# Kernel optimization log

Measured on AMD Instinct MI355X. Metric: run time of the kernel, lower is better.

The kernel has to match this reference:

```python
import jax, jax.numpy as jnp
import numpy as np


def setup_inputs() -> dict:
    key = jax.random.key(0)
    k0, k1, k2, k3 = jax.random.split(key, 4)
    B, S, D, F, E = 2, 2048, 1024, 4096, 8
    hidden_states = jax.random.normal(k0, (B, S, D), dtype=jnp.float32)
    Wr = jax.random.normal(k1, (E, D), dtype=jnp.float32) * 0.02   # router Linear weight [E, D]
    W1 = jax.random.normal(k2, (E, D, F), dtype=jnp.float32) * 0.02  # expert w1 (transposed torch layout)
    W2 = jax.random.normal(k3, (E, F, D), dtype=jnp.float32) * 0.02  # expert w2
    return {"hidden_states": hidden_states, "Wr": Wr, "W1": W1, "W2": W2, "top_k": 2}


def reference(hidden_states, Wr, W1, W2, top_k):
    # hidden_states: [B, S, D]; Wr: [E, D]; W1: [E, D, F]; W2: [E, F, D]
    E = Wr.shape[0]
    dt = hidden_states.dtype

    # Router: logits -> top-k expert indices. NOTE: the original module computes
    # softmax routing weights over the top-k logits but never applies them in the
    # combine step, so the output is an UNWEIGHTED sum over selected experts.
    router_logits = jnp.einsum('bsd,ed->bse', hidden_states, Wr)
    _, topk_idx = jax.lax.top_k(router_logits, top_k)            # [B, S, K]

    # mask[b,s,e] = 1 if expert e is in token (b,s)'s top-k (indices are distinct)
    mask = (jax.nn.one_hot(topk_idx, E, dtype=dt).sum(axis=-2) > 0).astype(dt)  # [B, S, E]

    # Dense per-expert FFN (SiLU MLP, no bias, dropout=identity in eval):
    h = jax.nn.silu(jnp.einsum('bsd,edf->bsef', hidden_states, W1))  # [B, S, E, F]
    y = jnp.einsum('bsef,efd->bsed', h, W2)                          # [B, S, E, D]

    # Combine: unweighted sum over selected experts (faithful to source)
    return jnp.einsum('bsed,bse->bsd', y, mask)
```

## Files before the change

### kernel.cpp

```cpp
#include <hip/hip_runtime.h>
#include <hip/hip_bf16.h>
#include <stdint.h>

#define TOKENS 4096
#define DDIM 1024
#define FDIM 4096
#define NEXP 8
#define BM 128
#define BN 256
#define BK 64
#define MT (TOKENS / BM)

typedef __attribute__((ext_vector_type(4))) float f32x4;
typedef __attribute__((ext_vector_type(8))) short short8;

__device__ __forceinline__ unsigned short f2bf(float f) {
    union { float f; uint32_t u; } v; v.f = f;
    uint32_t u = v.u;
    return (unsigned short)((u + 0x7fff + ((u >> 16) & 1)) >> 16);
}

#define BARRIER() asm volatile("s_barrier" ::: "memory")
#define WAIT_VM0() asm volatile("s_waitcnt vmcnt(0)" ::: "memory")
#define GLDS(SRC, DST) __builtin_amdgcn_global_load_lds( \
    (const __attribute__((address_space(1))) void*)(SRC), \
    (__attribute__((address_space(3))) void*)(DST), 16, 0, 0)

__global__ __launch_bounds__(256) void cvt_x(const float* __restrict__ x,
                                             unsigned short* __restrict__ xb, int n) {
    int i = (blockIdx.x * 256 + threadIdx.x) * 8;
    if (i >= n) return;
    float4 a = *(const float4*)(x + i);
    float4 b = *(const float4*)(x + i + 4);
    short8 o;
    o[0] = f2bf(a.x); o[1] = f2bf(a.y); o[2] = f2bf(a.z); o[3] = f2bf(a.w);
    o[4] = f2bf(b.x); o[5] = f2bf(b.y); o[6] = f2bf(b.z); o[7] = f2bf(b.w);
    *(short8*)(xb + i) = o;
}

__global__ __launch_bounds__(256) void transpose_cvt(const float* __restrict__ in,
                                                     unsigned short* __restrict__ out,
                                                     int R, int C) {
    __shared__ float tile[32][33];
    int e = blockIdx.z;
    int r0 = blockIdx.y * 32, c0 = blockIdx.x * 32;
    const float* src = in + (size_t)e * R * C;
    unsigned short* dst = out + (size_t)e * R * C;
    int t = threadIdx.x;
    int rr = t >> 3;
    int cc = (t & 7) * 4;
    float4 v = *(const float4*)(src + (size_t)(r0 + rr) * C + c0 + cc);
    tile[rr][cc + 0] = v.x; tile[rr][cc + 1] = v.y;
    tile[rr][cc + 2] = v.z; tile[rr][cc + 3] = v.w;
    __syncthreads();
    int oc = rr;
    int orr = cc;
    ushort4 o;
    o.x = f2bf(tile[orr + 0][oc]);
    o.y = f2bf(tile[orr + 1][oc]);
    o.z = f2bf(tile[orr + 2][oc]);
    o.w = f2bf(tile[orr + 3][oc]);
    *(ushort4*)(dst + (size_t)(c0 + oc) * R + r0 + orr) = o;
}

__global__ __launch_bounds__(256) void router(const float* __restrict__ x,
                                              const float* __restrict__ wr,
                                              int* __restrict__ cnt,
                                              int* __restrict__ list) {
    __shared__ float wl[NEXP * DDIM];
    int t = threadIdx.x;
    for (int i = t; i < NEXP * DDIM; i += 256) wl[i] = wr[i];
    __syncthreads();
    int tok = blockIdx.x * 4 + (t >> 6);
    int lane = t & 63;
    float acc[NEXP];
#pragma unroll
    for (int e = 0; e < NEXP; e++) acc[e] = 0.f;
    const float* xr = x + (size_t)tok * DDIM;
    for (int d = lane; d < DDIM; d += 64) {
        float xv = xr[d];
#pragma unroll
        for (int e = 0; e < NEXP; e++) acc[e] += xv * wl[e * DDIM + d];
    }
#pragma unroll
    for (int e = 0; e < NEXP; e++) {
#pragma unroll
        for (int off = 32; off; off >>= 1) acc[e] += __shfl_xor(acc[e], off);
    }
    if (lane == 0) {
        int e1 = 0; float v1 = acc[0];
        for (int e = 1; e < NEXP; e++) if (acc[e] > v1) { v1 = acc[e]; e1 = e; }
        int e2 = -1; float v2 = -1e30f;
        for (int e = 0; e < NEXP; e++) if (e != e1 && acc[e] > v2) { v2 = acc[e]; e2 = e; }
        int p1 = atomicAdd(&cnt[e1], 1);
        list[e1 * TOKENS + p1] = tok;
        int p2 = atomicAdd(&cnt[e2], 1);
        list[e2 * TOKENS + p2] = tok;
    }
}

__global__ void prefix(const int* __restrict__ cnt, int* __restrict__ off) {
    if (threadIdx.x == 0) {
        int s = 0;
        for (int e = 0; e < NEXP; e++) { off[e] = s; s += cnt[e]; }
    }
}

template <bool GATHER_A, bool SILU>
__global__ __launch_bounds__(512, 2) void gemm_moe2(
    const unsigned short* __restrict__ Abase,
    const unsigned short* __restrict__ Wt,
    const int* __restrict__ cnt, const int* __restrict__ off,
    const int* __restrict__ list,
    unsigned short* __restrict__ Hout,
    float* __restrict__ Yout,
    int KD, int NDIM) {
    __shared__ alignas(16) unsigned short As[2][BM * BK];
    __shared__ alignas(16) unsigned short Bs[2][BN * BK];

    int gx = gridDim.x;
    int flat = blockIdx.y * gx + blockIdx.x;
    int nwg = gx * (int)gridDim.y;
    int q = nwg >> 3, r = nwg & 7;
    int xcd = flat & 7, idx = flat >> 3;
    int swz = (xcd < r) ? (xcd * (q + 1) + idx) : (r * (q + 1) + (xcd - r) * q + idx);
    int bx = swz % gx, by = swz / gx;

    int e = bx / MT, mtile = bx % MT;
    int n_e = cnt[e];
    int m0 = mtile * BM;
    if (m0 >= n_e) return;
    int base = off[e];
    int n0 = by * BN;

    int t = threadIdx.x;
    int lane = t & 63;
    int wid = t >> 6;
    int wm = wid >> 2, wn = wid & 3;
    int r16 = lane & 15, g = lane >> 4;

    const unsigned short* pA[2];
    const unsigned short* pB[4];
    int ldsA[2], ldsB[4];
#pragma unroll
    for (int i = 0; i < 2; i++) {
        int c = i * 512 + t;
        int row = c >> 3, cc = c & 7;
        int arow = m0 + row; if (arow >= n_e) arow = n_e - 1;
        size_t grow = GATHER_A ? (size_t)list[e * TOKENS + arow] : (size_t)(base + arow);
        pA[i] = Abase + grow * (size_t)KD + ((cc ^ (row & 7)) << 3);
        ldsA[i] = c * 16;
    }
#pragma unroll
    for (int i = 0; i < 4; i++) {
        int c = i * 512 + t;
        int row = c >> 3, cc = c & 7;
        pB[i] = Wt + ((size_t)e * NDIM + n0 + row) * (size_t)KD + ((cc ^ (row & 7)) << 3);
        ldsB[i] = c * 16;
    }

    f32x4 acc[4][4];
#pragma unroll
    for (int i = 0; i < 4; i++)
#pragma unroll
        for (int j = 0; j < 4; j++) acc[i][j] = f32x4{0.f, 0.f, 0.f, 0.f};

#define FRAG(TILE, ROW, KC) (*(const short8*)&(TILE)[(ROW) * BK + ((((KC)) ^ ((ROW) & 7)) << 3)])

#pragma unroll
    for (int i = 0; i < 4; i++) { GLDS(pB[i], (char*)Bs[0] + ldsB[i]); pB[i] += BK; }
#pragma unroll
    for (int i = 0; i < 2; i++) { GLDS(pA[i], (char*)As[0] + ldsA[i]); pA[i] += BK; }
    WAIT_VM0();
    BARRIER();

    const int NT = KD / BK;
    for (int tk = 0; tk < NT; ++tk) {
        const unsigned short* Ac = As[tk & 1];
        const unsigned short* Bc = Bs[tk & 1];
        char* Ad = (char*)As[(tk & 1) ^ 1];
        char* Bd = (char*)Bs[(tk & 1) ^ 1];
        const bool pf = (tk + 1 < NT);

        short8 b0, b1, b2, b3, a0, a1;
        b0 = FRAG(Bc, wn * 64 + 0 * 16 + r16, g);
        b1 = FRAG(Bc, wn * 64 + 1 * 16 + r16, g);
        b2 = FRAG(Bc, wn * 64 + 2 * 16 + r16, g);
        b3 = FRAG(Bc, wn * 64 + 3 * 16 + r16, g);
        a0 = FRAG(Ac, wm * 64 + 0 * 16 + r16, g);
        a1 = FRAG(Ac, wm * 64 + 1 * 16 + r16, g);
        if (pf) { GLDS(pB[0], Bd + ldsB[0]); pB[0] += BK; GLDS(pB[1], Bd + ldsB[1]); pB[1] += BK; }
        BARRIER();
        __builtin_amdgcn_s_setprio(1);
        acc[0][0] = __builtin_amdgcn_mfma_f32_16x16x32_bf16(a0, b0, acc[0][0], 0, 0, 0);
        acc[0][1] = __builtin_amdgcn_mfma_f32_16x16x32_bf16(a0, b1, acc[0][1], 0, 0, 0);
        acc[0][2] = __builtin_amdgcn_mfma_f32_16x16x32_bf16(a0, b2, acc[0][2], 0, 0, 0);
        acc[0][3] = __builtin_amdgcn_mfma_f32_16x16x32_bf16(a0, b3, acc[0][3], 0, 0, 0);
        acc[1][0] = __builtin_amdgcn_mfma_f32_16x16x32_bf16(a1, b0, acc[1][0], 0, 0, 0);
        acc[1][1] = __builtin_amdgcn_mfma_f32_16x16x32_bf16(a1, b1, acc[1][1], 0, 0, 0);
        acc[1][2] = __builtin_amdgcn_mfma_f32_16x16x32_bf16(a1, b2, acc[1][2], 0, 0, 0);
        acc[1][3] = __builtin_amdgcn_mfma_f32_16x16x32_bf16(a1, b3, acc[1][3], 0, 0, 0);
        __builtin_amdgcn_s_setprio(0);
        BARRIER();
        a0 = FRAG(Ac, wm * 64 + 2 * 16 + r16, g);
        a1 = FRAG(Ac, wm * 64 + 3 * 16 + r16, g);
        if (pf) { GLDS(pB[2], Bd + ldsB[2]); pB[2] += BK; GLDS(pB[3], Bd + ldsB[3]); pB[3] += BK; }
        BARRIER();
        __builtin_amdgcn_s_setprio(1);
        acc[2][0] = __builtin_amdgcn_mfma_f32_16x16x32_bf16(a0, b0, acc[2][0], 0, 0, 0);
        acc[2][1] = __builtin_amdgcn_mfma_f32_16x16x32_bf16(a0, b1, acc[2][1], 0, 0, 0);
        acc[2][2] = __builtin_amdgcn_mfma_f32_16x16x32_bf16(a0, b2, acc[2][2], 0, 0, 0);
        acc[2][3] = __builtin_amdgcn_mfma_f32_16x16x32_bf16(a0, b3, acc[2][3], 0, 0, 0);
        acc[3][0] = __builtin_amdgcn_mfma_f32_16x16x32_bf16(a1, b0, acc[3][0], 0, 0, 0);
        acc[3][1] = __builtin_amdgcn_mfma_f32_16x16x32_bf16(a1, b1, acc[3][1], 0, 0, 0);
        acc[3][2] = __builtin_amdgcn_mfma_f32_16x16x32_bf16(a1, b2, acc[3][2], 0, 0, 0);
        acc[3][3] = __builtin_amdgcn_mfma_f32_16x16x32_bf16(a1, b3, acc[3][3], 0, 0, 0);
        __builtin_amdgcn_s_setprio(0);
        BARRIER();
        b0 = FRAG(Bc, wn * 64 + 0 * 16 + r16, 4 + g);
        b1 = FRAG(Bc, wn * 64 + 1 * 16 + r16, 4 + g);
        b2 = FRAG(Bc, wn * 64 + 2 * 16 + r16, 4 + g);
        b3 = FRAG(Bc, wn * 64 + 3 * 16 + r16, 4 + g);
        a0 = FRAG(Ac, wm * 64 + 0 * 16 + r16, 4 + g);
        a1 = FRAG(Ac, wm * 64 + 1 * 16 + r16, 4 + g);
        if (pf) { GLDS(pA[0], Ad + ldsA[0]); pA[0] += BK; GLDS(pA[1], Ad + ldsA[1]); pA[1] += BK; }
        BARRIER();
        __builtin_amdgcn_s_setprio(1);
        acc[0][0] = __builtin_amdgcn_mfma_f32_16x16x32_bf16(a0, b0, acc[0][0], 0, 0, 0);
        acc[0][1] = __builtin_amdgcn_mfma_f32_16x16x32_bf16(a0, b1, acc[0][1], 0, 0, 0);
        acc[0][2] = __builtin_amdgcn_mfma_f32_16x16x32_bf16(a0, b2, acc[0][2], 0, 0, 0);
        acc[0][3] = __builtin_amdgcn_mfma_f32_16x16x32_bf16(a0, b3, acc[0][3], 0, 0, 0);
        acc[1][0] = __builtin_amdgcn_mfma_f32_16x16x32_bf16(a1, b0, acc[1][0], 0, 0, 0);
        acc[1][1] = __builtin_amdgcn_mfma_f32_16x16x32_bf16(a1, b1, acc[1][1], 0, 0, 0);
        acc[1][2] = __builtin_amdgcn_mfma_f32_16x16x32_bf16(a1, b2, acc[1][2], 0, 0, 0);
        acc[1][3] = __builtin_amdgcn_mfma_f32_16x16x32_bf16(a1, b3, acc[1][3], 0, 0, 0);
        __builtin_amdgcn_s_setprio(0);
        BARRIER();
        a0 = FRAG(Ac, wm * 64 + 2 * 16 + r16, 4 + g);
        a1 = FRAG(Ac, wm * 64 + 3 * 16 + r16, 4 + g);
        BARRIER();
        __builtin_amdgcn_s_setprio(1);
        acc[2][0] = __builtin_amdgcn_mfma_f32_16x16x32_bf16(a0, b0, acc[2][0], 0, 0, 0);
        acc[2][1] = __builtin_amdgcn_mfma_f32_16x16x32_bf16(a0, b1, acc[2][1], 0, 0, 0);
        acc[2][2] = __builtin_amdgcn_mfma_f32_16x16x32_bf16(a0, b2, acc[2][2], 0, 0, 0);
        acc[2][3] = __builtin_amdgcn_mfma_f32_16x16x32_bf16(a0, b3, acc[2][3], 0, 0, 0);
        acc[3][0] = __builtin_amdgcn_mfma_f32_16x16x32_bf16(a1, b0, acc[3][0], 0, 0, 0);
        acc[3][1] = __builtin_amdgcn_mfma_f32_16x16x32_bf16(a1, b1, acc[3][1], 0, 0, 0);
        acc[3][2] = __builtin_amdgcn_mfma_f32_16x16x32_bf16(a1, b2, acc[3][2], 0, 0, 0);
        acc[3][3] = __builtin_amdgcn_mfma_f32_16x16x32_bf16(a1, b3, acc[3][3], 0, 0, 0);
        __builtin_amdgcn_s_setprio(0);
        if (pf) WAIT_VM0();
        BARRIER();
    }
#undef FRAG

#pragma unroll
    for (int mi = 0; mi < 4; ++mi) {
#pragma unroll
        for (int nj = 0; nj < 4; ++nj) {
#pragma unroll
            for (int qq = 0; qq < 4; ++qq) {
                int lr = wm * 64 + mi * 16 + g * 4 + qq;
                if (m0 + lr < n_e) {
                    int col = n0 + wn * 64 + nj * 16 + r16;
                    float v = acc[mi][nj][qq];
                    if (SILU) {
                        v = v / (1.f + __expf(-v));
                        Hout[(size_t)(base + m0 + lr) * NDIM + col] = f2bf(v);
                    } else {
                        int tok = list[e * TOKENS + m0 + lr];
                        atomicAdd(&Yout[(size_t)tok * NDIM + col], v);
                    }
                }
            }
        }
    }
}

extern "C" void kernel_launch(void* const* d_in, const int* in_sizes, int n_in,
                              void* d_out, int out_size, void* d_ws, size_t ws_size,
                              hipStream_t stream) {
    const float* X  = (const float*)d_in[0];
    const float* Wr = (const float*)d_in[1];
    const float* W1 = (const float*)d_in[2];
    const float* W2 = (const float*)d_in[3];
    float* Y = (float*)d_out;

    char* ws = (char*)d_ws;
    int* cnt  = (int*)(ws + 0);
    int* off  = (int*)(ws + 128);
    int* list = (int*)(ws + 1024);
    unsigned short* Xb = (unsigned short*)(ws + (1ull << 20));
    unsigned short* WT = (unsigned short*)(ws + (16ull << 20));
    unsigned short* H  = (unsigned short*)(ws + (80ull << 20));

    hipMemsetAsync(d_out, 0, (size_t)out_size * sizeof(float), stream);
    hipMemsetAsync(cnt, 0, 32, stream);

    cvt_x<<<TOKENS * DDIM / (256 * 8), 256, 0, stream>>>(X, Xb, TOKENS * DDIM);
    router<<<TOKENS / 4, 256, 0, stream>>>(X, Wr, cnt, list);
    prefix<<<1, 64, 0, stream>>>(cnt, off);

    transpose_cvt<<<dim3(FDIM / 32, DDIM / 32, NEXP), 256, 0, stream>>>(W1, WT, DDIM, FDIM);
    gemm_moe2<true, true><<<dim3(NEXP * MT, FDIM / BN), 512, 0, stream>>>(
        Xb, WT, cnt, off, list, H, nullptr, DDIM, FDIM);

    transpose_cvt<<<dim3(DDIM / 32, FDIM / 32, NEXP), 256, 0, stream>>>(W2, WT, FDIM, DDIM);
    gemm_moe2<false, false><<<dim3(NEXP * MT, DDIM / BN), 512, 0, stream>>>(
        H, WT, cnt, off, list, nullptr, Y, FDIM, DDIM);
}
```

Measured before the change: 542.7 us.

## Make MoE GEMMs persistent with an atomic work queue over non-empty tiles

Replaces the fixed 2D grid, where most blocks exit early on empty expert tiles, with 512 persistent workgroups. Each one pulls compact tile indices from an atomic counter, and a setup kernel precomputes per-expert tile bases and totals. The tile shrinks from 128x256 to 128x128 with 256 threads. The k-loop becomes simpler: all prefetches are issued at once and there is a single barrier per step. The intent is to remove launch waste and load imbalance. The costs are more weight-tile reloads, since N tiles are smaller, and less overlap between loads and MFMAs.

```diff
diff --git a/kernel.cpp b/kernel.cpp
--- a/kernel.cpp
+++ b/kernel.cpp
@@ -7,9 +7,8 @@
 #define FDIM 4096
 #define NEXP 8
 #define BM 128
-#define BN 256
+#define BN 128
 #define BK 64
-#define MT (TOKENS / BM)
 
 typedef __attribute__((ext_vector_type(4))) float f32x4;
 typedef __attribute__((ext_vector_type(8))) short short8;
@@ -99,182 +98,189 @@
     }
 }
 
-__global__ void prefix(const int* __restrict__ cnt, int* __restrict__ off) {
+__global__ void setup(const int* __restrict__ cnt, int* __restrict__ off,
+                      int* __restrict__ wbA, int* __restrict__ wbB,
+                      int* __restrict__ qctr, int* __restrict__ tot) {
     if (threadIdx.x == 0) {
-        int s = 0;
-        for (int e = 0; e < NEXP; e++) { off[e] = s; s += cnt[e]; }
+        int s = 0, ta = 0, tb = 0;
+        for (int e = 0; e < NEXP; e++) {
+            off[e] = s; s += cnt[e];
+            wbA[e] = ta; wbB[e] = tb;
+            int nt = (cnt[e] + BM - 1) / BM;
+            ta += nt * (FDIM / BN);
+            tb += nt * (DDIM / BN);
+        }
+        wbA[NEXP] = ta; wbB[NEXP] = tb;
+        tot[0] = ta; tot[1] = tb;
+        qctr[0] = 0; qctr[1] = 0;
     }
 }
 
 template <bool GATHER_A, bool SILU>
-__global__ __launch_bounds__(512, 2) void gemm_moe2(
+__global__ __launch_bounds__(256, 2) void gemm_moe3(
     const unsigned short* __restrict__ Abase,
     const unsigned short* __restrict__ Wt,
     const int* __restrict__ cnt, const int* __restrict__ off,
     const int* __restrict__ list,
+    const int* __restrict__ wbase,
+    int* __restrict__ qctr, const int* __restrict__ tot,
     unsigned short* __restrict__ Hout,
     float* __restrict__ Yout,
     int KD, int NDIM) {
     __shared__ alignas(16) unsigned short As[2][BM * BK];
     __shared__ alignas(16) unsigned short Bs[2][BN * BK];
-
-    int gx = gridDim.x;
-    int flat = blockIdx.y * gx + blockIdx.x;
-    int nwg = gx * (int)gridDim.y;
-    int q = nwg >> 3, r = nwg & 7;
-    int xcd = flat & 7, idx = flat >> 3;
-    int swz = (xcd < r) ? (xcd * (q + 1) + idx) : (r * (q + 1) + (xcd - r) * q + idx);
-    int bx = swz % gx, by = swz / gx;
-
-    int e = bx / MT, mtile = bx % MT;
-    int n_e = cnt[e];
-    int m0 = mtile * BM;
-    if (m0 >= n_e) return;
-    int base = off[e];
-    int n0 = by * BN;
+    __shared__ int wsh;
 
     int t = threadIdx.x;
     int lane = t & 63;
     int wid = t >> 6;
-    int wm = wid >> 2, wn = wid & 3;
+    int wm = wid >> 1, wn = wid & 1;
     int r16 = lane & 15, g = lane >> 4;
-
-    const unsigned short* pA[2];
-    const unsigned short* pB[4];
-    int ldsA[2], ldsB[4];
-#pragma unroll
-    for (int i = 0; i < 2; i++) {
-        int c = i * 512 + t;
-        int row = c >> 3, cc = c & 7;
-        int arow = m0 + row; if (arow >= n_e) arow = n_e - 1;
-        size_t grow = GATHER_A ? (size_t)list[e * TOKENS + arow] : (size_t)(base + arow);
-        pA[i] = Abase + grow * (size_t)KD + ((cc ^ (row & 7)) << 3);
-        ldsA[i] = c * 16;
-    }
-#pragma unroll
-    for (int i = 0; i < 4; i++) {
-        int c = i * 512 + t;
-        int row = c >> 3, cc = c & 7;
-        pB[i] = Wt + ((size_t)e * NDIM + n0 + row) * (size_t)KD + ((cc ^ (row & 7)) << 3);
-        ldsB[i] = c * 16;
-    }
-
-    f32x4 acc[4][4];
-#pragma unroll
-    for (int i = 0; i < 4; i++)
-#pragma unroll
-        for (int j = 0; j < 4; j++) acc[i][j] = f32x4{0.f, 0.f, 0.f, 0.f};
+    const int total = *tot;
 
 #define FRAG(TILE, ROW, KC) (*(const short8*)&(TILE)[(ROW) * BK + ((((KC)) ^ ((ROW) & 7)) << 3)])
 
-#pragma unroll
-    for (int i = 0; i < 4; i++) { GLDS(pB[i], (char*)Bs[0] + ldsB[i]); pB[i] += BK; }
-#pragma unroll
-    for (int i = 0; i < 2; i++) { GLDS(pA[i], (char*)As[0] + ldsA[i]); pA[i] += BK; }
-    WAIT_VM0();
-    BARRIER();
-
-    const int NT = KD / BK;
-    for (int tk = 0; tk < NT; ++tk) {
-        const unsigned short* Ac = As[tk & 1];
-        const unsigned short* Bc = Bs[tk & 1];
-        char* Ad = (char*)As[(tk & 1) ^ 1];
-        char* Bd = (char*)Bs[(tk & 1) ^ 1];
-        const bool pf = (tk + 1 < NT);
-
-        short8 b0, b1, b2, b3, a0, a1;
-        b0 = FRAG(Bc, wn * 64 + 0 * 16 + r16, g);
-        b1 = FRAG(Bc, wn * 64 + 1 * 16 + r16, g);
-        b2 = FRAG(Bc, wn * 64 + 2 * 16 + r16, g);
-        b3 = FRAG(Bc, wn * 64 + 3 * 16 + r16, g);
-        a0 = FRAG(Ac, wm * 64 + 0 * 16 + r16, g);
-        a1 = FRAG(Ac, wm * 64 + 1 * 16 + r16, g);
-        if (pf) { GLDS(pB[0], Bd + ldsB[0]); pB[0] += BK; GLDS(pB[1], Bd + ldsB[1]); pB[1] += BK; }
+    for (;;) {
+        if (t == 0) wsh = atomicAdd(qctr, 1);
+        __syncthreads();
+        int w = wsh;
+        if (w >= total) break;
+
+        int e = 0;
+        while (e < NEXP - 1 && w >= wbase[e + 1]) e++;
+        w -= wbase[e];
+        int n_e = cnt[e];
+        int ntm = (n_e + BM - 1) >> 7;
+        int by = w / ntm;
+        int mtile = w - by * ntm;
+        int m0 = mtile * BM;
+        int n0 = by * BN;
+        int base = off[e];
+
+        const unsigned short* pA[4];
+        const unsigned short* pB[4];
+        int ldsA[4], ldsB[4];
+#pragma unroll
+        for (int i = 0; i < 4; i++) {
+            int c = i * 256 + t;
+            int row = c >> 3, cc = c & 7;
+            int arow = m0 + row; if (arow >= n_e) arow = n_e - 1;
+            size_t grow = GATHER_A ? (size_t)list[e * TOKENS + arow] : (size_t)(base + arow);
+            pA[i] = Abase + grow * (size_t)KD + ((cc ^ (row & 7)) << 3);
+            ldsA[i] = c * 16;
+            pB[i] = Wt + ((size_t)e * NDIM + n0 + row) * (size_t)KD + ((cc ^ (row & 7)) << 3);
+            ldsB[i] = c * 16;
+        }
+
+        f32x4 acc[4][4];
+#pragma unroll
+        for (int i = 0; i < 4; i++)
+#pragma unroll
+            for (int j = 0; j < 4; j++) acc[i][j] = f32x4{0.f, 0.f, 0.f, 0.f};
+
+#pragma unroll
+        for (int i = 0; i < 4; i++) { GLDS(pB[i], (char*)Bs[0] + ldsB[i]); pB[i] += BK; }
+#pragma unroll
+        for (int i = 0; i < 4; i++) { GLDS(pA[i], (char*)As[0] + ldsA[i]); pA[i] += BK; }
+        WAIT_VM0();
         BARRIER();
-        __builtin_amdgcn_s_setprio(1);
-        acc[0][0] = __builtin_amdgcn_mfma_f32_16x16x32_bf16(a0, b0, acc[0][0], 0, 0, 0);
-        acc[0][1] = __builtin_amdgcn_mfma_f32_16x16x32_bf16(a0, b1, acc[0][1], 0, 0, 0);
-        acc[0][2] = __builtin_amdgcn_mfma_f32_16x16x32_bf16(a0, b2, acc[0][2], 0, 0, 0);
-        acc[0][3] = __builtin_amdgcn_mfma_f32_16x16x32_bf16(a0, b3, acc[0][3], 0, 0, 0);
-        acc[1][0] = __builtin_amdgcn_mfma_f32_16x16x32_bf16(a1, b0, acc[1][0], 0, 0, 0);
-        acc[1][1] = __builtin_amdgcn_mfma_f32_16x16x32_bf16(a1, b1, acc[1][1], 0, 0, 0);
-        acc[1][2] = __builtin_amdgcn_mfma_f32_16x16x32_bf16(a1, b2, acc[1][2], 0, 0, 0);
-        acc[1][3] = __builtin_amdgcn_mfma_f32_16x16x32_bf16(a1, b3, acc[1][3], 0, 0, 0);
-        __builtin_amdgcn_s_setprio(0);
-        BARRIER();
-        a0 = FRAG(Ac, wm * 64 + 2 * 16 + r16, g);
-        a1 = FRAG(Ac, wm * 64 + 3 * 16 + r16, g);
-        if (pf) { GLDS(pB[2], Bd + ldsB[2]); pB[2] += BK; GLDS(pB[3], Bd + ldsB[3]); pB[3] += BK; }
-        BARRIER();
-        __builtin_amdgcn_s_setprio(1);
-        acc[2][0] = __builtin_amdgcn_mfma_f32_16x16x32_bf16(a0, b0, acc[2][0], 0, 0, 0);
-        acc[2][1] = __builtin_amdgcn_mfma_f32_16x16x32_bf16(a0, b1, acc[2][1], 0, 0, 0);
-        acc[2][2] = __builtin_amdgcn_mfma_f32_16x16x32_bf16(a0, b2, acc[2][2], 0, 0, 0);
-        acc[2][3] = __builtin_amdgcn_mfma_f32_16x16x32_bf16(a0, b3, acc[2][3], 0, 0, 0);
-        acc[3][0] = __builtin_amdgcn_mfma_f32_16x16x32_bf16(a1, b0, acc[3][0], 0, 0, 0);
-        acc[3][1] = __builtin_amdgcn_mfma_f32_16x16x32_bf16(a1, b1, acc[3][1], 0, 0, 0);
-        acc[3][2] = __builtin_amdgcn_mfma_f32_16x16x32_bf16(a1, b2, acc[3][2], 0, 0, 0);
-        acc[3][3] = __builtin_amdgcn_mfma_f32_16x16x32_bf16(a1, b3, acc[3][3], 0, 0, 0);
-        __builtin_amdgcn_s_setprio(0);
-        BARRIER();
-        b0 = FRAG(Bc, wn * 64 + 0 * 16 + r16, 4 + g);
-        b1 = FRAG(Bc, wn * 64 + 1 * 16 + r16, 4 + g);
-        b2 = FRAG(Bc, wn * 64 + 2 * 16 + r16, 4 + g);
-        b3 = FRAG(Bc, wn * 64 + 3 * 16 + r16, 4 + g);
-        a0 = FRAG(Ac, wm * 64 + 0 * 16 + r16, 4 + g);
-        a1 = FRAG(Ac, wm * 64 + 1 * 16 + r16, 4 + g);
-        if (pf) { GLDS(pA[0], Ad + ldsA[0]); pA[0] += BK; GLDS(pA[1], Ad + ldsA[1]); pA[1] += BK; }
-        BARRIER();
-        __builtin_amdgcn_s_setprio(1);
-        acc[0][0] = __builtin_amdgcn_mfma_f32_16x16x32_bf16(a0, b0, acc[0][0], 0, 0, 0);
-        acc[0][1] = __builtin_amdgcn_mfma_f32_16x16x32_bf16(a0, b1, acc[0][1], 0, 0, 0);
-        acc[0][2] = __builtin_amdgcn_mfma_f32_16x16x32_bf16(a0, b2, acc[0][2], 0, 0, 0);
-        acc[0][3] = __builtin_amdgcn_mfma_f32_16x16x32_bf16(a0, b3, acc[0][3], 0, 0, 0);
-        acc[1][0] = __builtin_amdgcn_mfma_f32_16x16x32_bf16(a1, b0, acc[1][0], 0, 0, 0);
-        acc[1][1] = __builtin_amdgcn_mfma_f32_16x16x32_bf16(a1, b1, acc[1][1], 0, 0, 0);
-        acc[1][2] = __builtin_amdgcn_mfma_f32_16x16x32_bf16(a1, b2, acc[1][2], 0, 0, 0);
-        acc[1][3] = __builtin_amdgcn_mfma_f32_16x16x32_bf16(a1, b3, acc[1][3], 0, 0, 0);
-        __builtin_amdgcn_s_setprio(0);
-        BARRIER();
-        a0 = FRAG(Ac, wm * 64 + 2 * 16 + r16, 4 + g);
-        a1 = FRAG(Ac, wm * 64 + 3 * 16 + r16, 4 + g);
-        BARRIER();
-        __builtin_amdgcn_s_setprio(1);
-        acc[2][0] = __builtin_amdgcn_mfma_f32_16x16x32_bf16(a0, b0, acc[2][0], 0, 0, 0);
-        acc[2][1] = __builtin_amdgcn_mfma_f32_16x16x32_bf16(a0, b1, acc[2][1], 0, 0, 0);
-        acc[2][2] = __builtin_amdgcn_mfma_f32_16x16x32_bf16(a0, b2, acc[2][2], 0, 0, 0);
-        acc[2][3] = __builtin_amdgcn_mfma_f32_16x16x32_bf16(a0, b3, acc[2][3], 0, 0, 0);
-        acc[3][0] = __builtin_amdgcn_mfma_f32_16x16x32_bf16(a1, b0, acc[3][0], 0, 0, 0);
-        acc[3][1] = __builtin_amdgcn_mfma_f32_16x16x32_bf16(a1, b1, acc[3][1], 0, 0, 0);
-        acc[3][2] = __builtin_amdgcn_mfma_f32_16x16x32_bf16(a1, b2, acc[3][2], 0, 0, 0);
-        acc[3][3] = __builtin_amdgcn_mfma_f32_16x16x32_bf16(a1, b3, acc[3][3], 0, 0, 0);
-        __builtin_amdgcn_s_setprio(0);
-        if (pf) WAIT_VM0();
-        BARRIER();
-    }
-#undef FRAG
-
-#pragma unroll
-    for (int mi = 0; mi < 4; ++mi) {
-#pragma unroll
-        for (int nj = 0; nj < 4; ++nj) {
-#pragma unroll
-            for (int qq = 0; qq < 4; ++qq) {
-                int lr = wm * 64 + mi * 16 + g * 4 + qq;
-                if (m0 + lr < n_e) {
-                    int col = n0 + wn * 64 + nj * 16 + r16;
-                    float v = acc[mi][nj][qq];
-                    if (SILU) {
-                        v = v / (1.f + __expf(-v));
-                        Hout[(size_t)(base + m0 + lr) * NDIM + col] = f2bf(v);
-                    } else {
-                        int tok = list[e * TOKENS + m0 + lr];
-                        atomicAdd(&Yout[(size_t)tok * NDIM + col], v);
+
+        const int NT = KD / BK;
+        for (int tk = 0; tk < NT; ++tk) {
+            const unsigned short* Ac = As[tk & 1];
+            const unsigned short* Bc = Bs[tk & 1];
+            char* Ad = (char*)As[(tk & 1) ^ 1];
+            char* Bd = (char*)Bs[(tk & 1) ^ 1];
+            const bool pf = (tk + 1 < NT);
+
+            if (pf) {
+#pragma unroll
+                for (int i = 0; i < 4; i++) { GLDS(pB[i], Bd + ldsB[i]); pB[i] += BK; }
+#pragma unroll
+                for (int i = 0; i < 4; i++) { GLDS(pA[i], Ad + ldsA[i]); pA[i] += BK; }
+            }
+
+            short8 a0, a1, a2, a3, b0, b1, b2, b3;
+            a0 = FRAG(Ac, wm * 64 + 0 * 16 + r16, g);
+            a1 = FRAG(Ac, wm * 64 + 1 * 16 + r16, g);
+            a2 = FRAG(Ac, wm * 64 + 2 * 16 + r16, g);
+            a3 = FRAG(Ac, wm * 64 + 3 * 16 + r16, g);
+            b0 = FRAG(Bc, wn * 64 + 0 * 16 + r16, g);
+            b1 = FRAG(Bc, wn * 64 + 1 * 16 + r16, g);
+            b2 = FRAG(Bc, wn * 64 + 2 * 16 + r16, g);
+            b3 = FRAG(Bc, wn * 64 + 3 * 16 + r16, g);
+            __builtin_amdgcn_s_setprio(1);
+            acc[0][0] = __builtin_amdgcn_mfma_f32_16x16x32_bf16(a0, b0, acc[0][0], 0, 0, 0);
+            acc[0][1] = __builtin_amdgcn_mfma_f32_16x16x32_bf16(a0, b1, acc[0][1], 0, 0, 0);
+            acc[0][2] = __builtin_amdgcn_mfma_f32_16x16x32_bf16(a0, b2, acc[0][2], 0, 0, 0);
+            acc[0][3] = __builtin_amdgcn_mfma_f32_16x16x32_bf16(a0, b3, acc[0][3], 0, 0, 0);
+            acc[1][0] = __builtin_amdgcn_mfma_f32_16x16x32_bf16(a1, b0, acc[1][0], 0, 0, 0);
+            acc[1][1] = __builtin_amdgcn_mfma_f32_16x16x32_bf16(a1, b1, acc[1][1], 0, 0, 0);
+            acc[1][2] = __builtin_amdgcn_mfma_f32_16x16x32_bf16(a1, b2, acc[1][2], 0, 0, 0);
+            acc[1][3] = __builtin_amdgcn_mfma_f32_16x16x32_bf16(a1, b3, acc[1][3], 0, 0, 0);
+            acc[2][0] = __builtin_amdgcn_mfma_f32_16x16x32_bf16(a2, b0, acc[2][0], 0, 0, 0);
+            acc[2][1] = __builtin_amdgcn_mfma_f32_16x16x32_bf16(a2, b1, acc[2][1], 0, 0, 0);
+            acc[2][2] = __builtin_amdgcn_mfma_f32_16x16x32_bf16(a2, b2, acc[2][2], 0, 0, 0);
+            acc[2][3] = __builtin_amdgcn_mfma_f32_16x16x32_bf16(a2, b3, acc[2][3], 0, 0, 0);
+            acc[3][0] = __builtin_amdgcn_mfma_f32_16x16x32_bf16(a3, b0, acc[3][0], 0, 0, 0);
+            acc[3][1] = __builtin_amdgcn_mfma_f32_16x16x32_bf16(a3, b1, acc[3][1], 0, 0, 0);
+            acc[3][2] = __builtin_amdgcn_mfma_f32_16x16x32_bf16(a3, b2, acc[3][2], 0, 0, 0);
+            acc[3][3] = __builtin_amdgcn_mfma_f32_16x16x32_bf16(a3, b3, acc[3][3], 0, 0, 0);
+            __builtin_amdgcn_s_setprio(0);
+            a0 = FRAG(Ac, wm * 64 + 0 * 16 + r16, 4 + g);
+            a1 = FRAG(Ac, wm * 64 + 1 * 16 + r16, 4 + g);
+            a2 = FRAG(Ac, wm * 64 + 2 * 16 + r16, 4 + g);
+            a3 = FRAG(Ac, wm * 64 + 3 * 16 + r16, 4 + g);
+            b0 = FRAG(Bc, wn * 64 + 0 * 16 + r16, 4 + g);
+            b1 = FRAG(Bc, wn * 64 + 1 * 16 + r16, 4 + g);
+            b2 = FRAG(Bc, wn * 64 + 2 * 16 + r16, 4 + g);
+            b3 = FRAG(Bc, wn * 64 + 3 * 16 + r16, 4 + g);
+            __builtin_amdgcn_s_setprio(1);
+            acc[0][0] = __builtin_amdgcn_mfma_f32_16x16x32_bf16(a0, b0, acc[0][0], 0, 0, 0);
+            acc[0][1] = __builtin_amdgcn_mfma_f32_16x16x32_bf16(a0, b1, acc[0][1], 0, 0, 0);
+            acc[0][2] = __builtin_amdgcn_mfma_f32_16x16x32_bf16(a0, b2, acc[0][2], 0, 0, 0);
+            acc[0][3] = __builtin_amdgcn_mfma_f32_16x16x32_bf16(a0, b3, acc[0][3], 0, 0, 0);
+            acc[1][0] = __builtin_amdgcn_mfma_f32_16x16x32_bf16(a1, b0, acc[1][0], 0, 0, 0);
+            acc[1][1] = __builtin_amdgcn_mfma_f32_16x16x32_bf16(a1, b1, acc[1][1], 0, 0, 0);
+            acc[1][2] = __builtin_amdgcn_mfma_f32_16x16x32_bf16(a1, b2, acc[1][2], 0, 0, 0);
+            acc[1][3] = __builtin_amdgcn_mfma_f32_16x16x32_bf16(a1, b3, acc[1][3], 0, 0, 0);
+            acc[2][0] = __builtin_amdgcn_mfma_f32_16x16x32_bf16(a2, b0, acc[2][0], 0, 0, 0);
+            acc[2][1] = __builtin_amdgcn_mfma_f32_16x16x32_bf16(a2, b1, acc[2][1], 0, 0, 0);
+            acc[2][2] = __builtin_amdgcn_mfma_f32_16x16x32_bf16(a2, b2, acc[2][2], 0, 0, 0);
+            acc[2][3] = __builtin_amdgcn_mfma_f32_16x16x32_bf16(a2, b3, acc[2][3], 0, 0, 0);
+            acc[3][0] = __builtin_amdgcn_mfma_f32_16x16x32_bf16(a3, b0, acc[3][0], 0, 0, 0);
+            acc[3][1] = __builtin_amdgcn_mfma_f32_16x16x32_bf16(a3, b1, acc[3][1], 0, 0, 0);
+            acc[3][2] = __builtin_amdgcn_mfma_f32_16x16x32_bf16(a3, b2, acc[3][2], 0, 0, 0);
+            acc[3][3] = __builtin_amdgcn_mfma_f32_16x16x32_bf16(a3, b3, acc[3][3], 0, 0, 0);
+            __builtin_amdgcn_s_setprio(0);
+
+            if (pf) WAIT_VM0();
+            BARRIER();
+        }
+
+#pragma unroll
+        for (int mi = 0; mi < 4; ++mi) {
+#pragma unroll
+            for (int nj = 0; nj < 4; ++nj) {
+#pragma unroll
+                for (int qq = 0; qq < 4; ++qq) {
+                    int lr = wm * 64 + mi * 16 + g * 4 + qq;
+                    if (m0 + lr < n_e) {
+                        int col = n0 + wn * 64 + nj * 16 + r16;
+                        float v = acc[mi][nj][qq];
+                        if (SILU) {
+                            v = v / (1.f + __expf(-v));
+                            Hout[(size_t)(base + m0 + lr) * NDIM + col] = f2bf(v);
+                        } else {
+                            int tok = list[e * TOKENS + m0 + lr];
+                            atomicAdd(&Yout[(size_t)tok * NDIM + col], v);
+                        }
                     }
                 }
             }
         }
     }
+#undef FRAG
 }
 
 extern "C" void kernel_launch(void* const* d_in, const int* in_sizes, int n_in,
@@ -288,7 +294,11 @@
 
     char* ws = (char*)d_ws;
     int* cnt  = (int*)(ws + 0);
-    int* off  = (int*)(ws + 128);
+    int* off  = (int*)(ws + 64);
+    int* wbA  = (int*)(ws + 128);
+    int* wbB  = (int*)(ws + 192);
+    int* qctr = (int*)(ws + 256);
+    int* tot  = (int*)(ws + 288);
     int* list = (int*)(ws + 1024);
     unsigned short* Xb = (unsigned short*)(ws + (1ull << 20));
     unsigned short* WT = (unsigned short*)(ws + (16ull << 20));
@@ -299,13 +309,13 @@
 
     cvt_x<<<TOKENS * DDIM / (256 * 8), 256, 0, stream>>>(X, Xb, TOKENS * DDIM);
     router<<<TOKENS / 4, 256, 0, stream>>>(X, Wr, cnt, list);
-    prefix<<<1, 64, 0, stream>>>(cnt, off);
+    setup<<<1, 64, 0, stream>>>(cnt, off, wbA, wbB, qctr, tot);
 
     transpose_cvt<<<dim3(FDIM / 32, DDIM / 32, NEXP), 256, 0, stream>>>(W1, WT, DDIM, FDIM);
-    gemm_moe2<true, true><<<dim3(NEXP * MT, FDIM / BN), 512, 0, stream>>>(
-        Xb, WT, cnt, off, list, H, nullptr, DDIM, FDIM);
+    gemm_moe3<true, true><<<512, 256, 0, stream>>>(
+        Xb, WT, cnt, off, list, wbA, qctr + 0, tot + 0, H, nullptr, DDIM, FDIM);
 
     transpose_cvt<<<dim3(DDIM / 32, FDIM / 32, NEXP), 256, 0, stream>>>(W2, WT, FDIM, DDIM);
-    gemm_moe2<false, false><<<dim3(NEXP * MT, DDIM / BN), 512, 0, stream>>>(
-        H, WT, cnt, off, list, nullptr, Y, FDIM, DDIM);
-}
+    gemm_moe3<false, false><<<512, 256, 0, stream>>>(
+        H, WT, cnt, off, list, wbB, qctr + 1, tot + 1, nullptr, Y, FDIM, DDIM);
+}
```

New measurement: 492.1 us. 1.1x faster.
